# Performance work log

Hardware: AMD Instinct MI355X
Metric: run time of the kernel (lower is better)

The kernel has to match this reference:

```python
import jax, jax.numpy as jnp
import numpy as np

N_NODES = 100000
N_EDGES = 600000
N_GRAPHS = 256
D_IN, D_HID, N_CLS = 256, 128, 10
LEAKY_SLOPE = 0.01  # torch default


def gcn_conv(x, W, b, row, col, edge_weight, num_nodes):
    # PyG gcn_norm with add_self_loops=False:
    # deg[j] = sum of edge_weight into target j; norm = d^-1/2[row] * w * d^-1/2[col]
    deg = jax.ops.segment_sum(edge_weight, col, num_segments=num_nodes)
    dis = jnp.where(deg > 0, jax.lax.rsqrt(jnp.where(deg > 0, deg, 1.0)), 0.0)
    norm = dis[row] * edge_weight * dis[col]
    h = x @ W                                   # [N, H] dense GEMM first (as GCNConv does)
    msg = norm[:, None] * h[row]                # [E, H] gather + scale
    out = jax.ops.segment_sum(msg, col, num_segments=num_nodes)  # scatter-add
    return out + b


def setup_inputs() -> dict:
    key = jax.random.key(0)
    ks = jax.random.split(key, 10)
    x = jax.random.normal(ks[0], (N_NODES, D_IN), dtype=jnp.float32)
    edge_index = jax.random.randint(ks[1], (2, N_EDGES), 0, N_NODES, dtype=jnp.int64)
    edge_weight = jax.random.uniform(ks[2], (N_EDGES,), dtype=jnp.float32)
    batch = jnp.sort(jax.random.randint(ks[3], (N_NODES,), 0, N_GRAPHS, dtype=jnp.int64))
    s1 = 1.0 / np.sqrt(D_IN)
    s2 = 1.0 / np.sqrt(D_HID)
    W1 = jax.random.uniform(ks[4], (D_IN, D_HID), jnp.float32, -s1, s1)
    b1 = jnp.zeros((D_HID,), jnp.float32)
    W2 = jax.random.uniform(ks[5], (D_HID, D_HID), jnp.float32, -s2, s2)
    b2 = jnp.zeros((D_HID,), jnp.float32)
    Wl = jax.random.uniform(ks[6], (D_HID, N_CLS), jnp.float32, -s2, s2)
    bl = jax.random.uniform(ks[7], (N_CLS,), jnp.float32, -s2, s2)
    return {"x": x, "edge_index": edge_index, "edge_weight": edge_weight, "batch": batch,
            "W1": W1, "b1": b1, "W2": W2, "b2": b2, "Wl": Wl, "bl": bl}


def reference(x, edge_index, edge_weight, batch, W1, b1, W2, b2, Wl, bl):
    # Eval-mode forward: dropout is identity (training=False).
    row, col = edge_index[0], edge_index[1]
    h = gcn_conv(x, W1, b1, row, col, edge_weight, N_NODES)
    h = jnp.where(h >= 0, h, LEAKY_SLOPE * h)
    h = gcn_conv(h, W2, b2, row, col, edge_weight, N_NODES)
    h = jnp.where(h >= 0, h, LEAKY_SLOPE * h)
    # global mean pool over graphs
    sums = jax.ops.segment_sum(h, batch, num_segments=N_GRAPHS)          # [G, H]
    cnts = jax.ops.segment_sum(jnp.ones((h.shape[0],), h.dtype), batch, num_segments=N_GRAPHS)
    pooled = sums / jnp.maximum(cnts, 1.0)[:, None]
    logits = pooled @ Wl + bl
    return jax.nn.log_softmax(logits, axis=1)
```

## Files before the change

kernel.cpp:

```cpp
#include <hip/hip_runtime.h>

typedef float f32x4 __attribute__((ext_vector_type(4)));
typedef short bf16x8 __attribute__((ext_vector_type(8)));

#define SLOPE 0.01f
#define BKT 64

__device__ __forceinline__ short f2bf(float f) {
    unsigned int u = __float_as_uint(f);
    unsigned int r = (u + 0x7fffu + ((u >> 16) & 1u)) >> 16;
    return (short)r;
}

__global__ void k_init(const float* __restrict__ W1, const float* __restrict__ W2,
                       short* __restrict__ wf1, short* __restrict__ wf2,
                       int* __restrict__ cnt,
                       float* __restrict__ sums, float* __restrict__ cnts, int N, int G) {
    int t = blockIdx.x * blockDim.x + threadIdx.x;
    if (t < 4096) {
        int ntile = t >> 9;
        int ks = (t >> 6) & 7;
        int lane = t & 63;
        int h = lane >> 4, c = lane & 15;
#pragma unroll
        for (int j = 0; j < 8; j++) {
            int k = ks * 32 + h * 8 + j;
            wf1[t * 8 + j] = f2bf(W1[k * 128 + ntile * 16 + c]);
        }
    } else if (t < 6144) {
        int s = t - 4096;
        int ntile = s >> 8;
        int ks = (s >> 6) & 3;
        int lane = s & 63;
        int h = lane >> 4, c = lane & 15;
#pragma unroll
        for (int j = 0; j < 8; j++) {
            int k = ks * 32 + h * 8 + j;
            wf2[s * 8 + j] = f2bf(W2[k * 128 + ntile * 16 + c]);
        }
    } else {
        long u = t - 6144;
        if (u < N) cnt[u] = 0;
        else {
            long v = u - N;
            if (v < (long)G * 128) sums[v] = 0.f;
            else if (v < (long)G * 128 + G) cnts[v - (long)G * 128] = 0.f;
        }
    }
}

__global__ __launch_bounds__(256, 3) void k_gemm1_hist(
        const float* __restrict__ Av, const short* __restrict__ Wf,
        ushort* __restrict__ out, int M, int gemmBlocks,
        const int* __restrict__ ei, const float* __restrict__ ew,
        int* __restrict__ cnt, uint2* __restrict__ ebuf,
        int E, int histBlocks) {
    __shared__ short lds[4 * 8 * 64 * 8];
    const int tid = threadIdx.x;
    int b = blockIdx.x;
    int nInter = 2 * (gemmBlocks < histBlocks ? gemmBlocks : histBlocks);
    bool isGemm; int idx;
    if (b < nInter) { isGemm = (b & 1) == 0; idx = b >> 1; }
    else {
        int r = b - nInter;
        if (gemmBlocks < histBlocks) { isGemm = false; idx = gemmBlocks + r; }
        else                         { isGemm = true;  idx = histBlocks + r; }
    }

    if (!isGemm) {
        int base = idx * 256 + tid;
        int stride = histBlocks * 256;
        int iv[4]; bool av[4]; int cv[4]; int rv[4]; float wv2[4]; int pv[4];
#pragma unroll
        for (int k = 0; k < 4; k++) { iv[k] = base + k * stride; av[k] = iv[k] < E; }
#pragma unroll
        for (int k = 0; k < 4; k++) if (av[k]) cv[k] = ei[E + iv[k]];
#pragma unroll
        for (int k = 0; k < 4; k++) if (av[k]) { rv[k] = ei[iv[k]]; wv2[k] = ew[iv[k]]; }
#pragma unroll
        for (int k = 0; k < 4; k++) if (av[k]) pv[k] = atomicAdd(&cnt[cv[k]], 1);
#pragma unroll
        for (int k = 0; k < 4; k++)
            if (av[k] && pv[k] < BKT)
                ebuf[(long)cv[k] * BKT + pv[k]] = make_uint2((unsigned)rv[k], __float_as_uint(wv2[k]));
        return;
    }

    const int lane = tid & 63;
    const int wid = tid >> 6;
    const int h = lane >> 4, c = lane & 15;
    const int rowW = idx * 128 + wid * 32;

    bf16x8 afr[2][8];
#pragma unroll
    for (int rg = 0; rg < 2; rg++) {
        int arow = rowW + rg * 16 + c;
        if (arow >= M) arow = M - 1;
        const float* arp = Av + (long)arow * 256 + h * 8;
#pragma unroll
        for (int ks = 0; ks < 8; ks++) {
            float4 a0 = *(const float4*)(arp + ks * 32);
            float4 a1 = *(const float4*)(arp + ks * 32 + 4);
            bf16x8 f;
            f[0] = f2bf(a0.x); f[1] = f2bf(a0.y); f[2] = f2bf(a0.z); f[3] = f2bf(a0.w);
            f[4] = f2bf(a1.x); f[5] = f2bf(a1.y); f[6] = f2bf(a1.z); f[7] = f2bf(a1.w);
            afr[rg][ks] = f;
        }
    }

    const bf16x8* lf8 = (const bf16x8*)lds;
#pragma unroll
    for (int half = 0; half < 2; half++) {
        if (half) __syncthreads();
        {
            const float4* wsrc = (const float4*)Wf + half * 2048;
            float4* wdst = (float4*)lds;
#pragma unroll
            for (int i = 0; i < 8; i++)
                wdst[i * 256 + tid] = wsrc[i * 256 + tid];
        }
        __syncthreads();
#pragma unroll
        for (int ntl = 0; ntl < 4; ntl++) {
            int nt = half * 4 + ntl;
            bf16x8 bfr[8];
#pragma unroll
            for (int ks = 0; ks < 8; ks++)
                bfr[ks] = lf8[(ntl * 8 + ks) * 64 + lane];
            f32x4 acc0 = {0.f, 0.f, 0.f, 0.f}, acc1 = {0.f, 0.f, 0.f, 0.f};
#pragma unroll
            for (int ks = 0; ks < 8; ks++) {
                acc0 = __builtin_amdgcn_mfma_f32_16x16x32_bf16(bfr[ks], afr[0][ks], acc0, 0, 0, 0);
                acc1 = __builtin_amdgcn_mfma_f32_16x16x32_bf16(bfr[ks], afr[1][ks], acc1, 0, 0, 0);
            }
#pragma unroll
            for (int rg = 0; rg < 2; rg++) {
                f32x4 acc = rg ? acc1 : acc0;
                int orow = rowW + rg * 16 + c;
                if (orow < M) {
                    ushort4 pk;
                    pk.x = (ushort)f2bf(acc[0]); pk.y = (ushort)f2bf(acc[1]);
                    pk.z = (ushort)f2bf(acc[2]); pk.w = (ushort)f2bf(acc[3]);
                    *(ushort4*)(out + (long)orow * 128 + nt * 16 + h * 4) = pk;
                }
            }
        }
    }
}

__global__ void k_degdis(const int* __restrict__ cnt, const uint2* __restrict__ ebuf,
                         float* __restrict__ dis, int N) {
    int gid = blockIdx.x * blockDim.x + threadIdx.x;
    int n = gid >> 3, e = gid & 7;
    if (n >= N) return;
    int m = cnt[n];
    const uint2* p = ebuf + (long)n * BKT;
    float d = 0.f;
    for (int i = e; i < m; i += 8) d += __uint_as_float(p[i].y);
    d += __shfl_xor(d, 1);
    d += __shfl_xor(d, 2);
    d += __shfl_xor(d, 4);
    if (e == 0) dis[n] = d > 0.f ? rsqrtf(d) : 0.f;
}

__global__ void k_norm(const int* __restrict__ cnt, const float* __restrict__ dis,
                       uint2* __restrict__ ebuf, int N) {
    int gid = blockIdx.x * blockDim.x + threadIdx.x;
    int n = gid >> 3, e = gid & 7;
    if (n >= N) return;
    int m = cnt[n];
    float dc = dis[n];
    uint2* p = ebuf + (long)n * BKT;
    for (int i = e; i < m; i += 8) {
        uint2 v = p[i];
        float nr = dis[v.x] * __uint_as_float(v.y) * dc;
        p[i].y = __float_as_uint(nr);
    }
}

__global__ __launch_bounds__(256, 4) void k_gemm2(const ushort* __restrict__ Av,
                                                  const short* __restrict__ Wf,
                                                  ushort* __restrict__ out, int M) {
    __shared__ short lds[4 * 8 * 64 * 8];
    const int tid = threadIdx.x;
    {
        const float4* wsrc = (const float4*)Wf;
        float4* wdst = (float4*)lds;
#pragma unroll
        for (int i = 0; i < 8; i++)
            wdst[i * 256 + tid] = wsrc[i * 256 + tid];
    }
    __syncthreads();

    const int lane = tid & 63;
    const int wid = tid >> 6;
    const int h = lane >> 4, c = lane & 15;
    const int rowW = blockIdx.x * 128 + wid * 32;

    bf16x8 afr[2][4];
#pragma unroll
    for (int rg = 0; rg < 2; rg++) {
        int arow = rowW + rg * 16 + c;
        if (arow >= M) arow = M - 1;
        const ushort* arp = Av + (long)arow * 128 + h * 8;
#pragma unroll
        for (int ks = 0; ks < 4; ks++)
            afr[rg][ks] = *(const bf16x8*)(arp + ks * 32);
    }

    const bf16x8* lf8 = (const bf16x8*)lds;
#pragma unroll
    for (int nt = 0; nt < 8; nt++) {
        bf16x8 bfr[4];
#pragma unroll
        for (int ks = 0; ks < 4; ks++)
            bfr[ks] = lf8[(nt * 4 + ks) * 64 + lane];
        f32x4 acc0 = {0.f, 0.f, 0.f, 0.f}, acc1 = {0.f, 0.f, 0.f, 0.f};
#pragma unroll
        for (int ks = 0; ks < 4; ks++) {
            acc0 = __builtin_amdgcn_mfma_f32_16x16x32_bf16(bfr[ks], afr[0][ks], acc0, 0, 0, 0);
            acc1 = __builtin_amdgcn_mfma_f32_16x16x32_bf16(bfr[ks], afr[1][ks], acc1, 0, 0, 0);
        }
#pragma unroll
        for (int rg = 0; rg < 2; rg++) {
            f32x4 acc = rg ? acc1 : acc0;
            int orow = rowW + rg * 16 + c;
            if (orow < M) {
                ushort4 pk;
                pk.x = (ushort)f2bf(acc[0]); pk.y = (ushort)f2bf(acc[1]);
                pk.z = (ushort)f2bf(acc[2]); pk.w = (ushort)f2bf(acc[3]);
                *(ushort4*)(out + (long)orow * 128 + nt * 16 + h * 4) = pk;
            }
        }
    }
}

template <int OM>
__global__ __launch_bounds__(256) void k_agg(const uint2* __restrict__ ebuf,
                                             const int* __restrict__ cnt,
                                             const unsigned* __restrict__ hbuf,
                                             unsigned* __restrict__ outp, const float* __restrict__ bias, int N) {
    int wv = (blockIdx.x * blockDim.x + threadIdx.x) >> 6;
    int lane = threadIdx.x & 63;
    if (wv >= N) return;
    long s = (long)wv * BKT;
    int m = cnt[wv];
    float ax = 0.f, ay = 0.f;
    for (int base = 0; base < m; base += 16) {
        int rem = m - base;
        int nact = rem < 16 ? rem : 16;
        uint2 p = make_uint2(0u, 0u);
        if (lane < nact) p = ebuf[s + base + lane];
        int px = (int)p.x, py = (int)p.y;
#pragma unroll
        for (int j = 0; j < 8; j++) {
            unsigned rj = (unsigned)__shfl(px, j);
            float nj = __uint_as_float((unsigned)__shfl(py, j));
            unsigned hv = hbuf[(long)rj * 64 + lane];
            ax = fmaf(nj, __uint_as_float(hv << 16), ax);
            ay = fmaf(nj, __uint_as_float(hv & 0xffff0000u), ay);
        }
        if (rem > 8) {
#pragma unroll
            for (int j = 8; j < 16; j++) {
                unsigned rj = (unsigned)__shfl(px, j);
                float nj = __uint_as_float((unsigned)__shfl(py, j));
                unsigned hv = hbuf[(long)rj * 64 + lane];
                ax = fmaf(nj, __uint_as_float(hv << 16), ax);
                ay = fmaf(nj, __uint_as_float(hv & 0xffff0000u), ay);
            }
        }
    }
    float vx = ax, vy = ay;
    if (OM == 0) {
        float2 bv = ((const float2*)bias)[lane];
        vx += bv.x; vx = vx < 0.f ? SLOPE * vx : vx;
        vy += bv.y; vy = vy < 0.f ? SLOPE * vy : vy;
    }
    unsigned pk = (unsigned)(ushort)f2bf(vx) | ((unsigned)(ushort)f2bf(vy) << 16);
    outp[(long)wv * 64 + lane] = pk;
}

__global__ __launch_bounds__(64) void k_pool(const unsigned* __restrict__ aggb, const float* __restrict__ b2,
                                             const int* __restrict__ batch, float* __restrict__ sums,
                                             float* __restrict__ cnts, int N) {
    int n0 = blockIdx.x * 128;
    if (n0 >= N) return;
    int t = threadIdx.x;
    float2 bv = ((const float2*)b2)[t];
    int end = min(n0 + 128, N);
    int curg = batch[n0];
    float ax = 0.f, ay = 0.f;
    int run = 0;
    for (int n = n0; n < end; n++) {
        int g = batch[n];
        if (g != curg) {
            atomicAdd(&sums[curg * 128 + 2 * t], ax);
            atomicAdd(&sums[curg * 128 + 2 * t + 1], ay);
            if (t == 0) atomicAdd(&cnts[curg], (float)run);
            ax = ay = 0.f; run = 0; curg = g;
        }
        unsigned pk = aggb[(long)n * 64 + t];
        float vx = __uint_as_float(pk << 16) + bv.x;        vx = vx < 0.f ? SLOPE * vx : vx;
        float vy = __uint_as_float(pk & 0xffff0000u) + bv.y; vy = vy < 0.f ? SLOPE * vy : vy;
        ax += vx; ay += vy; run++;
    }
    atomicAdd(&sums[curg * 128 + 2 * t], ax);
    atomicAdd(&sums[curg * 128 + 2 * t + 1], ay);
    if (t == 0) atomicAdd(&cnts[curg], (float)run);
}

__global__ void k_final(const float* __restrict__ sums, const float* __restrict__ cnts,
                        const float* __restrict__ Wl, const float* __restrict__ bl,
                        float* __restrict__ out, int G) {
    int g = blockIdx.x * blockDim.x + threadIdx.x;
    if (g >= G) return;
    float inv = 1.f / fmaxf(cnts[g], 1.f);
    float l[10];
#pragma unroll
    for (int c = 0; c < 10; c++) l[c] = bl[c];
    for (int k = 0; k < 128; k++) {
        float p = sums[g * 128 + k] * inv;
#pragma unroll
        for (int c = 0; c < 10; c++) l[c] += p * Wl[k * 10 + c];
    }
    float m = l[0];
#pragma unroll
    for (int c = 1; c < 10; c++) m = fmaxf(m, l[c]);
    float s = 0.f;
#pragma unroll
    for (int c = 0; c < 10; c++) s += expf(l[c] - m);
    float lse = m + logf(s);
#pragma unroll
    for (int c = 0; c < 10; c++) out[g * 10 + c] = l[c] - lse;
}

extern "C" void kernel_launch(void* const* d_in, const int* in_sizes, int n_in,
                              void* d_out, int out_size, void* d_ws, size_t ws_size,
                              hipStream_t stream) {
    const float* x  = (const float*)d_in[0];
    const int*   ei = (const int*)d_in[1];
    const float* ew = (const float*)d_in[2];
    const int*   batch = (const int*)d_in[3];
    const float* W1 = (const float*)d_in[4];
    const float* b1 = (const float*)d_in[5];
    const float* W2 = (const float*)d_in[6];
    const float* b2 = (const float*)d_in[7];
    const float* Wl = (const float*)d_in[8];
    const float* bl = (const float*)d_in[9];
    float* out = (float*)d_out;

    const int N = in_sizes[0] / 256;
    const int E = in_sizes[2];
    const int G = out_size / 10;

    char* ws = (char*)d_ws;
    float*  dis  = (float*)(ws);
    int*    cnt  = (int*)  (ws + 400384);
    uint2*  ebuf = (uint2*)(ws + 800768);
    ushort* hbuf = (ushort*)(ws + 52000768);
    ushort* abuf = (ushort*)(ws + 77600768);
    short*  wf1  = (short*)(ws + 103200768);
    short*  wf2  = (short*)(ws + 103266304);
    float*  sums = (float*)(ws + 103299072);
    float*  cnts = (float*)(ws + 103430144);

    long initThreads = 6144 + (long)N + (long)G * 128 + G;
    int initBlocks = (int)((initThreads + 255) / 256);
    k_init<<<initBlocks, 256, 0, stream>>>(W1, W2, wf1, wf2, cnt, sums, cnts, N, G);

    const int GB = (N + 127) / 128;
    const int HB = (E + 1023) / 1024;
    k_gemm1_hist<<<GB + HB, 256, 0, stream>>>(x, wf1, hbuf, N, GB,
                                              ei, ew, cnt, ebuf, E, HB);

    k_degdis<<<(N * 8 + 255) / 256, 256, 0, stream>>>(cnt, ebuf, dis, N);
    k_norm<<<(N * 8 + 255) / 256, 256, 0, stream>>>(cnt, dis, ebuf, N);

    k_agg<0><<<(N + 3) / 4, 256, 0, stream>>>(ebuf, cnt, (const unsigned*)hbuf, (unsigned*)abuf, b1, N);
    k_gemm2<<<(N + 127) / 128, 256, 0, stream>>>(abuf, wf2, hbuf, N);
    k_agg<1><<<(N + 3) / 4, 256, 0, stream>>>(ebuf, cnt, (const unsigned*)hbuf, (unsigned*)abuf, nullptr, N);

    k_pool<<<(N + 127) / 128, 64, 0, stream>>>((const unsigned*)abuf, b2, batch, sums, cnts, N);
    k_final<<<1, 256, 0, stream>>>(sums, cnts, Wl, bl, out, G);
}
```

Measured before the change: 195.6 us.

## Merge degree and norm passes, fold pool and final head via last-block flag

The degree and norm kernels become one pass. It stores w*dis[col] per edge, and the aggregation kernels now multiply by dis[row], gathered per edge, when they read the edge buffer. The pooling kernel and the final linear/log-softmax kernel are also fused: an atomic completion counter lets the last block compute the logits. This removes two launches and one full read/write pass over the edge buffer. In exchange it adds a random dis gather in both aggregation passes and a serialized tail on a single 64-thread block.

Measured after the change: 235.8 us. +20.5%, slower.

```diff
diff --git a/kernel.cpp b/kernel.cpp
--- a/kernel.cpp
+++ b/kernel.cpp
@@ -15,7 +15,8 @@
 __global__ void k_init(const float* __restrict__ W1, const float* __restrict__ W2,
                        short* __restrict__ wf1, short* __restrict__ wf2,
                        int* __restrict__ cnt,
-                       float* __restrict__ sums, float* __restrict__ cnts, int N, int G) {
+                       float* __restrict__ sums, float* __restrict__ cnts,
+                       int* __restrict__ done, int N, int G) {
     int t = blockIdx.x * blockDim.x + threadIdx.x;
     if (t < 4096) {
         int ntile = t >> 9;
@@ -45,6 +46,7 @@
             long v = u - N;
             if (v < (long)G * 128) sums[v] = 0.f;
             else if (v < (long)G * 128 + G) cnts[v - (long)G * 128] = 0.f;
+            else if (v == (long)G * 128 + G) *done = 0;
         }
     }
 }
@@ -148,33 +150,30 @@
     }
 }
 
-__global__ void k_degdis(const int* __restrict__ cnt, const uint2* __restrict__ ebuf,
-                         float* __restrict__ dis, int N) {
+__global__ void k_dn(const int* __restrict__ cnt, uint2* __restrict__ ebuf,
+                     float* __restrict__ dis, int N) {
     int gid = blockIdx.x * blockDim.x + threadIdx.x;
     int n = gid >> 3, e = gid & 7;
     if (n >= N) return;
-    int m = cnt[n];
-    const uint2* p = ebuf + (long)n * BKT;
+    int m = min(cnt[n], BKT);
+    uint2* p = ebuf + (long)n * BKT;
+    float wv[8];
     float d = 0.f;
-    for (int i = e; i < m; i += 8) d += __uint_as_float(p[i].y);
+#pragma unroll
+    for (int k = 0; k < 8; k++) {
+        int i = e + k * 8;
+        wv[k] = 0.f;
+        if (i < m) { wv[k] = __uint_as_float(p[i].y); d += wv[k]; }
+    }
     d += __shfl_xor(d, 1);
     d += __shfl_xor(d, 2);
     d += __shfl_xor(d, 4);
-    if (e == 0) dis[n] = d > 0.f ? rsqrtf(d) : 0.f;
-}
-
-__global__ void k_norm(const int* __restrict__ cnt, const float* __restrict__ dis,
-                       uint2* __restrict__ ebuf, int N) {
-    int gid = blockIdx.x * blockDim.x + threadIdx.x;
-    int n = gid >> 3, e = gid & 7;
-    if (n >= N) return;
-    int m = cnt[n];
-    float dc = dis[n];
-    uint2* p = ebuf + (long)n * BKT;
-    for (int i = e; i < m; i += 8) {
-        uint2 v = p[i];
-        float nr = dis[v.x] * __uint_as_float(v.y) * dc;
-        p[i].y = __float_as_uint(nr);
+    float di = d > 0.f ? rsqrtf(d) : 0.f;
+    if (e == 0) dis[n] = di;
+#pragma unroll
+    for (int k = 0; k < 8; k++) {
+        int i = e + k * 8;
+        if (i < m) p[i].y = __float_as_uint(wv[k] * di);
     }
 }
 
@@ -237,25 +236,27 @@
 
 template <int OM>
 __global__ __launch_bounds__(256) void k_agg(const uint2* __restrict__ ebuf,
-                                             const int* __restrict__ cnt,
+                                             const int* __restrict__ cnt, const float* __restrict__ dis,
                                              const unsigned* __restrict__ hbuf,
                                              unsigned* __restrict__ outp, const float* __restrict__ bias, int N) {
     int wv = (blockIdx.x * blockDim.x + threadIdx.x) >> 6;
     int lane = threadIdx.x & 63;
     if (wv >= N) return;
     long s = (long)wv * BKT;
-    int m = cnt[wv];
+    int m = min(cnt[wv], BKT);
     float ax = 0.f, ay = 0.f;
     for (int base = 0; base < m; base += 16) {
         int rem = m - base;
         int nact = rem < 16 ? rem : 16;
         uint2 p = make_uint2(0u, 0u);
-        if (lane < nact) p = ebuf[s + base + lane];
-        int px = (int)p.x, py = (int)p.y;
+        float dr = 0.f;
+        if (lane < nact) { p = ebuf[s + base + lane]; dr = dis[p.x]; }
+        float nrmL = dr * __uint_as_float(p.y);
+        int px = (int)p.x;
 #pragma unroll
         for (int j = 0; j < 8; j++) {
             unsigned rj = (unsigned)__shfl(px, j);
-            float nj = __uint_as_float((unsigned)__shfl(py, j));
+            float nj = __shfl(nrmL, j);
             unsigned hv = hbuf[(long)rj * 64 + lane];
             ax = fmaf(nj, __uint_as_float(hv << 16), ax);
             ay = fmaf(nj, __uint_as_float(hv & 0xffff0000u), ay);
@@ -264,7 +265,7 @@
 #pragma unroll
             for (int j = 8; j < 16; j++) {
                 unsigned rj = (unsigned)__shfl(px, j);
-                float nj = __uint_as_float((unsigned)__shfl(py, j));
+                float nj = __shfl(nrmL, j);
                 unsigned hv = hbuf[(long)rj * 64 + lane];
                 ax = fmaf(nj, __uint_as_float(hv << 16), ax);
                 ay = fmaf(nj, __uint_as_float(hv & 0xffff0000u), ay);
@@ -281,58 +282,67 @@
     outp[(long)wv * 64 + lane] = pk;
 }
 
-__global__ __launch_bounds__(64) void k_pool(const unsigned* __restrict__ aggb, const float* __restrict__ b2,
-                                             const int* __restrict__ batch, float* __restrict__ sums,
-                                             float* __restrict__ cnts, int N) {
+__global__ __launch_bounds__(64) void k_poolfinal(
+        const unsigned* __restrict__ aggb, const float* __restrict__ b2,
+        const int* __restrict__ batch, float* __restrict__ sums, float* __restrict__ cnts,
+        const float* __restrict__ Wl, const float* __restrict__ bl,
+        float* __restrict__ out, int* __restrict__ done, int N, int G) {
     int n0 = blockIdx.x * 128;
-    if (n0 >= N) return;
     int t = threadIdx.x;
-    float2 bv = ((const float2*)b2)[t];
-    int end = min(n0 + 128, N);
-    int curg = batch[n0];
-    float ax = 0.f, ay = 0.f;
-    int run = 0;
-    for (int n = n0; n < end; n++) {
-        int g = batch[n];
-        if (g != curg) {
-            atomicAdd(&sums[curg * 128 + 2 * t], ax);
-            atomicAdd(&sums[curg * 128 + 2 * t + 1], ay);
-            if (t == 0) atomicAdd(&cnts[curg], (float)run);
-            ax = ay = 0.f; run = 0; curg = g;
-        }
-        unsigned pk = aggb[(long)n * 64 + t];
-        float vx = __uint_as_float(pk << 16) + bv.x;        vx = vx < 0.f ? SLOPE * vx : vx;
-        float vy = __uint_as_float(pk & 0xffff0000u) + bv.y; vy = vy < 0.f ? SLOPE * vy : vy;
-        ax += vx; ay += vy; run++;
-    }
-    atomicAdd(&sums[curg * 128 + 2 * t], ax);
-    atomicAdd(&sums[curg * 128 + 2 * t + 1], ay);
-    if (t == 0) atomicAdd(&cnts[curg], (float)run);
-}
-
-__global__ void k_final(const float* __restrict__ sums, const float* __restrict__ cnts,
-                        const float* __restrict__ Wl, const float* __restrict__ bl,
-                        float* __restrict__ out, int G) {
-    int g = blockIdx.x * blockDim.x + threadIdx.x;
-    if (g >= G) return;
-    float inv = 1.f / fmaxf(cnts[g], 1.f);
-    float l[10];
-#pragma unroll
-    for (int c = 0; c < 10; c++) l[c] = bl[c];
-    for (int k = 0; k < 128; k++) {
-        float p = sums[g * 128 + k] * inv;
-#pragma unroll
-        for (int c = 0; c < 10; c++) l[c] += p * Wl[k * 10 + c];
-    }
-    float m = l[0];
-#pragma unroll
-    for (int c = 1; c < 10; c++) m = fmaxf(m, l[c]);
-    float s = 0.f;
-#pragma unroll
-    for (int c = 0; c < 10; c++) s += expf(l[c] - m);
-    float lse = m + logf(s);
-#pragma unroll
-    for (int c = 0; c < 10; c++) out[g * 10 + c] = l[c] - lse;
+    if (n0 < N) {
+        float2 bv = ((const float2*)b2)[t];
+        int end = min(n0 + 128, N);
+        int curg = batch[n0];
+        float ax = 0.f, ay = 0.f;
+        int run = 0;
+        for (int n = n0; n < end; n++) {
+            int g = batch[n];
+            if (g != curg) {
+                atomicAdd(&sums[curg * 128 + 2 * t], ax);
+                atomicAdd(&sums[curg * 128 + 2 * t + 1], ay);
+                if (t == 0) atomicAdd(&cnts[curg], (float)run);
+                ax = ay = 0.f; run = 0; curg = g;
+            }
+            unsigned pk = aggb[(long)n * 64 + t];
+            float vx = __uint_as_float(pk << 16) + bv.x;        vx = vx < 0.f ? SLOPE * vx : vx;
+            float vy = __uint_as_float(pk & 0xffff0000u) + bv.y; vy = vy < 0.f ? SLOPE * vy : vy;
+            ax += vx; ay += vy; run++;
+        }
+        atomicAdd(&sums[curg * 128 + 2 * t], ax);
+        atomicAdd(&sums[curg * 128 + 2 * t + 1], ay);
+        if (t == 0) atomicAdd(&cnts[curg], (float)run);
+    }
+
+    __shared__ int lastflag;
+    if (t == 0) {
+        __threadfence();
+        int r = atomicAdd(done, 1);
+        lastflag = (r == (int)gridDim.x - 1) ? 1 : 0;
+    }
+    __syncthreads();
+    if (!lastflag) return;
+    __threadfence();
+    for (int g = t; g < G; g += 64) {
+        float cv = __hip_atomic_load(&cnts[g], __ATOMIC_RELAXED, __HIP_MEMORY_SCOPE_AGENT);
+        float inv = 1.f / fmaxf(cv, 1.f);
+        float l[10];
+#pragma unroll
+        for (int c = 0; c < 10; c++) l[c] = bl[c];
+        for (int k = 0; k < 128; k++) {
+            float p = __hip_atomic_load(&sums[g * 128 + k], __ATOMIC_RELAXED, __HIP_MEMORY_SCOPE_AGENT) * inv;
+#pragma unroll
+            for (int c = 0; c < 10; c++) l[c] += p * Wl[k * 10 + c];
+        }
+        float mx = l[0];
+#pragma unroll
+        for (int c = 1; c < 10; c++) mx = fmaxf(mx, l[c]);
+        float s = 0.f;
+#pragma unroll
+        for (int c = 0; c < 10; c++) s += expf(l[c] - mx);
+        float lse = mx + logf(s);
+#pragma unroll
+        for (int c = 0; c < 10; c++) out[g * 10 + c] = l[c] - lse;
+    }
 }
 
 extern "C" void kernel_launch(void* const* d_in, const int* in_sizes, int n_in,
@@ -357,6 +367,7 @@
     char* ws = (char*)d_ws;
     float*  dis  = (float*)(ws);
     int*    cnt  = (int*)  (ws + 400384);
+    int*    done = (int*)  (ws + 800384);
     uint2*  ebuf = (uint2*)(ws + 800768);
     ushort* hbuf = (ushort*)(ws + 52000768);
     ushort* abuf = (ushort*)(ws + 77600768);
@@ -365,22 +376,21 @@
     float*  sums = (float*)(ws + 103299072);
     float*  cnts = (float*)(ws + 103430144);
 
-    long initThreads = 6144 + (long)N + (long)G * 128 + G;
+    long initThreads = 6144 + (long)N + (long)G * 128 + G + 1;
     int initBlocks = (int)((initThreads + 255) / 256);
-    k_init<<<initBlocks, 256, 0, stream>>>(W1, W2, wf1, wf2, cnt, sums, cnts, N, G);
+    k_init<<<initBlocks, 256, 0, stream>>>(W1, W2, wf1, wf2, cnt, sums, cnts, done, N, G);
 
     const int GB = (N + 127) / 128;
     const int HB = (E + 1023) / 1024;
     k_gemm1_hist<<<GB + HB, 256, 0, stream>>>(x, wf1, hbuf, N, GB,
                                               ei, ew, cnt, ebuf, E, HB);
 
-    k_degdis<<<(N * 8 + 255) / 256, 256, 0, stream>>>(cnt, ebuf, dis, N);
-    k_norm<<<(N * 8 + 255) / 256, 256, 0, stream>>>(cnt, dis, ebuf, N);
-
-    k_agg<0><<<(N + 3) / 4, 256, 0, stream>>>(ebuf, cnt, (const unsigned*)hbuf, (unsigned*)abuf, b1, N);
+    k_dn<<<(N * 8 + 255) / 256, 256, 0, stream>>>(cnt, ebuf, dis, N);
+
+    k_agg<0><<<(N + 3) / 4, 256, 0, stream>>>(ebuf, cnt, dis, (const unsigned*)hbuf, (unsigned*)abuf, b1, N);
     k_gemm2<<<(N + 127) / 128, 256, 0, stream>>>(abuf, wf2, hbuf, N);
-    k_agg<1><<<(N + 3) / 4, 256, 0, stream>>>(ebuf, cnt, (const unsigned*)hbuf, (unsigned*)abuf, nullptr, N);
-
-    k_pool<<<(N + 127) / 128, 64, 0, stream>>>((const unsigned*)abuf, b2, batch, sums, cnts, N);
-    k_final<<<1, 256, 0, stream>>>(sums, cnts, Wl, bl, out, G);
-}
+    k_agg<1><<<(N + 3) / 4, 256, 0, stream>>>(ebuf, cnt, dis, (const unsigned*)hbuf, (unsigned*)abuf, nullptr, N);
+
+    k_poolfinal<<<(N + 127) / 128, 64, 0, stream>>>((const unsigned*)abuf, b2, batch,
+                                                    sums, cnts, Wl, bl, out, done, N, G);
+}
```
